# Performance work log

Hardware: AMD Instinct MI355X
Metric: run time of the kernel (lower is better)

Reference implementation:

```python
import jax, jax.numpy as jnp
import numpy as np

# Each of the 16 binary logic gates, relaxed to real values, is a multilinear
# function: gate(a,b) = c0 + c1*a + c2*b + c3*a*b. Rows follow the standard
# difflogic ordering: FALSE, AND, a&~b, a, ~a&b, b, XOR, OR, NOR, XNOR,
# ~b, a|~b, ~a, ~a|b, NAND, TRUE.
GATE_COEF = jnp.array([
    [0.0,  0.0,  0.0,  0.0],   # 0:  false
    [0.0,  0.0,  0.0,  1.0],   # 1:  a AND b
    [0.0,  1.0,  0.0, -1.0],   # 2:  a AND NOT b
    [0.0,  1.0,  0.0,  0.0],   # 3:  a
    [0.0,  0.0,  1.0, -1.0],   # 4:  NOT a AND b
    [0.0,  0.0,  1.0,  0.0],   # 5:  b
    [0.0,  1.0,  1.0, -2.0],   # 6:  a XOR b
    [0.0,  1.0,  1.0, -1.0],   # 7:  a OR b
    [1.0, -1.0, -1.0,  1.0],   # 8:  NOR
    [1.0, -1.0, -1.0,  2.0],   # 9:  XNOR
    [1.0,  0.0, -1.0,  0.0],   # 10: NOT b
    [1.0,  0.0, -1.0,  1.0],   # 11: a OR NOT b
    [1.0, -1.0,  0.0,  0.0],   # 12: NOT a
    [1.0, -1.0,  0.0,  1.0],   # 13: NOT a OR b
    [1.0,  0.0,  0.0, -1.0],   # 14: NAND
    [1.0,  0.0,  0.0,  0.0],   # 15: true
], dtype=jnp.float32)

B, IN_DIM, HIDDEN, N_LAYERS, OUT_DIM, TAU = 4096, 1024, 8192, 6, 8, 10.0
NPO = HIDDEN // OUT_DIM  # neurons_per_output


def logic_layer(h, w, ia, ib):
    # h: [B, in_dim]; w: [H, 16]; ia, ib: [H] int indices into in_dim.
    # Softmax-weighted blend of 16 gates == multilinear form with blended coefs.
    p = jax.nn.softmax(w, axis=-1)          # [H, 16]
    c = p @ GATE_COEF                       # [H, 4]
    a = h[:, ia]                            # [B, H] gather
    b = h[:, ib]                            # [B, H] gather
    return c[:, 0] + c[:, 1] * a + c[:, 2] * b + c[:, 3] * (a * b)


def setup_inputs() -> dict:
    key = jax.random.key(0)
    ks = jax.random.split(key, 8)
    return {
        "x": jax.random.uniform(ks[0], (B, IN_DIM), dtype=jnp.float32),
        "logic_w": jax.random.normal(ks[1], (N_LAYERS, HIDDEN, 16), dtype=jnp.float32),
        "scaler_w": jax.random.normal(ks[2], (OUT_DIM, OUT_DIM), dtype=jnp.float32) * 0.1,
        "scaler_b": jax.random.normal(ks[3], (OUT_DIM,), dtype=jnp.float32) * 0.1,
        "idx0_a": jax.random.randint(ks[4], (HIDDEN,), 0, IN_DIM, dtype=jnp.int32),
        "idx0_b": jax.random.randint(ks[5], (HIDDEN,), 0, IN_DIM, dtype=jnp.int32),
        "idx_a": jax.random.randint(ks[6], (N_LAYERS - 1, HIDDEN), 0, HIDDEN, dtype=jnp.int32),
        "idx_b": jax.random.randint(ks[7], (N_LAYERS - 1, HIDDEN), 0, HIDDEN, dtype=jnp.int32),
    }


def reference(x, logic_w, scaler_w, scaler_b, idx0_a, idx0_b, idx_a, idx_b):
    h = (x.reshape(x.shape[0], -1) > 0.5).astype(jnp.float32)   # binarize
    h = logic_layer(h, logic_w[0], idx0_a, idx0_b)               # [B, HIDDEN]
    for i in range(N_LAYERS - 1):
        h = logic_layer(h, logic_w[i + 1], idx_a[i], idx_b[i])
    h = h.reshape(h.shape[0], OUT_DIM, NPO)                      # [B, O, NPO]
    values = jnp.sum(h, axis=2) / TAU                            # [B, O]
    q_values = values @ scaler_w.T + scaler_b                    # nn.Linear
    return q_values
```

## Files before the change

kernel.cpp:

```cpp
#include <hip/hip_runtime.h>
#include <hip/hip_fp16.h>

constexpr int BATCH    = 4096;
constexpr int IN_DIM   = 1024;
constexpr int HIDDEN   = 8192;
constexpr int N_LAYERS = 6;
constexpr int OUT_DIM  = 8;
constexpr float INV_TAU = 0.1f;

constexpr int TB   = 4;
constexpr int NTH  = 1024;
constexpr int NPT  = HIDDEN / NTH;
constexpr int NWAVES = NTH / 64;

__device__ __forceinline__ uint2 pack4(float4 v) {
    __half2 lo = __float22half2_rn(make_float2(v.x, v.y));
    __half2 hi = __float22half2_rn(make_float2(v.z, v.w));
    uint2 r;
    r.x = *(const unsigned int*)&lo;
    r.y = *(const unsigned int*)&hi;
    return r;
}
__device__ __forceinline__ float4 unpack4(uint2 p) {
    __half2 lo = *(const __half2*)&p.x;
    __half2 hi = *(const __half2*)&p.y;
    float2 a = __half22float2(lo);
    float2 b = __half22float2(hi);
    return make_float4(a.x, a.y, b.x, b.y);
}

__global__ void prep_kernel(const float* __restrict__ logic_w,
                            const int* __restrict__ idx0_a,
                            const int* __restrict__ idx0_b,
                            const int* __restrict__ idx_a,
                            const int* __restrict__ idx_b,
                            uint2* __restrict__ coefp,
                            unsigned int* __restrict__ idxp, int n)
{
    int id = blockIdx.x * blockDim.x + threadIdx.x;
    if (id >= n) return;
    const int l = id / HIDDEN;
    const int j = id - l * HIDDEN;

    int ia, ib;
    if (l == 0) { ia = idx0_a[j]; ib = idx0_b[j]; }
    else        { ia = idx_a[(size_t)(l - 1) * HIDDEN + j];
                  ib = idx_b[(size_t)(l - 1) * HIDDEN + j]; }
    idxp[id] = (unsigned int)ia | ((unsigned int)ib << 16);

    const float4* w4 = (const float4*)(logic_w + (size_t)id * 16);
    float4 wa = w4[0], wb = w4[1], wc = w4[2], wd = w4[3];
    float wv[16] = {wa.x, wa.y, wa.z, wa.w, wb.x, wb.y, wb.z, wb.w,
                    wc.x, wc.y, wc.z, wc.w, wd.x, wd.y, wd.z, wd.w};
    float m = wv[0];
#pragma unroll
    for (int i = 1; i < 16; ++i) m = fmaxf(m, wv[i]);
    float e[16];
    float s = 0.f;
#pragma unroll
    for (int i = 0; i < 16; ++i) { e[i] = expf(wv[i] - m); s += e[i]; }
    float inv = 1.f / s;
    const float G0[16] = {0,0,0,0,0,0,0,0, 1,1,1,1,1,1,1,1};
    const float G1[16] = {0,0,1,1,0,0,1,1, -1,-1,0,0,-1,-1,0,0};
    const float G2[16] = {0,0,0,0,1,1,1,1, -1,-1,-1,-1,0,0,0,0};
    const float G3[16] = {0,1,-1,0,-1,0,-2,-1, 1,2,0,1,0,1,-1,0};
    float c0 = 0.f, c1 = 0.f, c2 = 0.f, c3 = 0.f;
#pragma unroll
    for (int i = 0; i < 16; ++i) {
        float p = e[i] * inv;
        c0 = fmaf(p, G0[i], c0);
        c1 = fmaf(p, G1[i], c1);
        c2 = fmaf(p, G2[i], c2);
        c3 = fmaf(p, G3[i], c3);
    }
    coefp[id] = pack4(make_float4(c0, c1, c2, c3));
}

__device__ __forceinline__ float4 gate4(float4 a, float4 b, float4 c) {
    float4 r;
    r.x = fmaf(c.w, a.x * b.x, fmaf(c.z, b.x, fmaf(c.y, a.x, c.x)));
    r.y = fmaf(c.w, a.y * b.y, fmaf(c.z, b.y, fmaf(c.y, a.y, c.x)));
    r.z = fmaf(c.w, a.z * b.z, fmaf(c.z, b.z, fmaf(c.y, a.z, c.x)));
    r.w = fmaf(c.w, a.w * b.w, fmaf(c.z, b.w, fmaf(c.y, a.w, c.x)));
    return r;
}

__global__ __launch_bounds__(NTH) void net_kernel(
    const float*  __restrict__ x,
    const uint2*  __restrict__ coefp,
    const unsigned int* __restrict__ idxp,
    const float*  __restrict__ scaler_w, const float* __restrict__ scaler_b,
    float* __restrict__ out)
{
    __shared__ uint2 h[HIDDEN];
    __shared__ uint2 hx[IN_DIM];
    __shared__ float4 warr[NWAVES];
    __shared__ float  vals[TB][OUT_DIM];

    const int tid = threadIdx.x;
    const int b0  = blockIdx.x * TB;

    {
        float4 xv;
        xv.x = (x[(size_t)(b0 + 0) * IN_DIM + tid] > 0.5f) ? 1.f : 0.f;
        xv.y = (x[(size_t)(b0 + 1) * IN_DIM + tid] > 0.5f) ? 1.f : 0.f;
        xv.z = (x[(size_t)(b0 + 2) * IN_DIM + tid] > 0.5f) ? 1.f : 0.f;
        xv.w = (x[(size_t)(b0 + 3) * IN_DIM + tid] > 0.5f) ? 1.f : 0.f;
        hx[tid] = pack4(xv);
    }
    __syncthreads();

    uint2 acc[NPT];

#pragma unroll
    for (int k = 0; k < NPT; ++k) {
        int j = k * NTH + tid;
        unsigned int pr = idxp[j];
        float4 a = unpack4(hx[pr & 0xffffu]);
        float4 b = unpack4(hx[pr >> 16]);
        float4 c = unpack4(coefp[j]);
        acc[k] = pack4(gate4(a, b, c));
    }
#pragma unroll
    for (int k = 0; k < NPT; ++k) h[k * NTH + tid] = acc[k];
    __syncthreads();

    for (int l = 1; l < N_LAYERS; ++l) {
        const unsigned int* ip = idxp  + (size_t)l * HIDDEN;
        const uint2*        cp = coefp + (size_t)l * HIDDEN;
#pragma unroll
        for (int k = 0; k < NPT; ++k) {
            int j = k * NTH + tid;
            unsigned int pr = ip[j];
            float4 a = unpack4(h[pr & 0xffffu]);
            float4 b = unpack4(h[pr >> 16]);
            float4 c = unpack4(cp[j]);
            acc[k] = pack4(gate4(a, b, c));
        }
        __syncthreads();
#pragma unroll
        for (int k = 0; k < NPT; ++k) h[k * NTH + tid] = acc[k];
        __syncthreads();
    }

    {
        const int k    = tid >> 7;
        const int base = k * 1024 + (tid & 127);
        float4 v = make_float4(0.f, 0.f, 0.f, 0.f);
#pragma unroll
        for (int i = 0; i < 8; ++i) {
            float4 t = unpack4(h[base + 128 * i]);
            v.x += t.x; v.y += t.y; v.z += t.z; v.w += t.w;
        }
#pragma unroll
        for (int off = 32; off > 0; off >>= 1) {
            v.x += __shfl_down(v.x, off);
            v.y += __shfl_down(v.y, off);
            v.z += __shfl_down(v.z, off);
            v.w += __shfl_down(v.w, off);
        }
        if ((tid & 63) == 0) warr[tid >> 6] = v;
    }
    __syncthreads();
    if (tid < OUT_DIM) {
        float4 a = warr[2 * tid], b = warr[2 * tid + 1];
        vals[0][tid] = (a.x + b.x) * INV_TAU;
        vals[1][tid] = (a.y + b.y) * INV_TAU;
        vals[2][tid] = (a.z + b.z) * INV_TAU;
        vals[3][tid] = (a.w + b.w) * INV_TAU;
    }
    __syncthreads();
    if (tid < TB * OUT_DIM) {
        int t  = tid >> 3;
        int oo = tid & 7;
        float q = scaler_b[oo];
#pragma unroll
        for (int o2 = 0; o2 < OUT_DIM; ++o2)
            q = fmaf(vals[t][o2], scaler_w[oo * OUT_DIM + o2], q);
        out[(size_t)(b0 + t) * OUT_DIM + oo] = q;
    }
}

extern "C" void kernel_launch(void* const* d_in, const int* in_sizes, int n_in,
                              void* d_out, int out_size, void* d_ws, size_t ws_size,
                              hipStream_t stream)
{
    const float* x        = (const float*)d_in[0];
    const float* logic_w  = (const float*)d_in[1];
    const float* scaler_w = (const float*)d_in[2];
    const float* scaler_b = (const float*)d_in[3];
    const int*   idx0_a   = (const int*)d_in[4];
    const int*   idx0_b   = (const int*)d_in[5];
    const int*   idx_a    = (const int*)d_in[6];
    const int*   idx_b    = (const int*)d_in[7];
    float* out = (float*)d_out;

    const int n = N_LAYERS * HIDDEN;
    uint2*        coefp = (uint2*)d_ws;
    unsigned int* idxp  = (unsigned int*)((char*)d_ws + (size_t)n * sizeof(uint2));

    prep_kernel<<<(n + 255) / 256, 256, 0, stream>>>(logic_w, idx0_a, idx0_b,
                                                     idx_a, idx_b, coefp, idxp, n);
    net_kernel<<<BATCH / TB, NTH, 0, stream>>>(x, coefp, idxp,
                                               scaler_w, scaler_b, out);
}
```

Before: 129.4 us.

## Compute gates in packed half2 and assign contiguous neurons per thread with vector loads

Measured after the change: 131.0 us. Within noise of the previous version (+1.2%).

```diff
diff --git a/kernel.cpp b/kernel.cpp
--- a/kernel.cpp
+++ b/kernel.cpp
@@ -13,19 +13,21 @@
 constexpr int NPT  = HIDDEN / NTH;
 constexpr int NWAVES = NTH / 64;
 
+__device__ __forceinline__ __half2 u2h(unsigned int u) {
+    union { unsigned int u; __half2 h; } v; v.u = u; return v.h;
+}
+__device__ __forceinline__ unsigned int h2u(__half2 h) {
+    union { unsigned int u; __half2 h; } v; v.h = h; return v.u;
+}
+
 __device__ __forceinline__ uint2 pack4(float4 v) {
     __half2 lo = __float22half2_rn(make_float2(v.x, v.y));
     __half2 hi = __float22half2_rn(make_float2(v.z, v.w));
-    uint2 r;
-    r.x = *(const unsigned int*)&lo;
-    r.y = *(const unsigned int*)&hi;
-    return r;
+    uint2 r; r.x = h2u(lo); r.y = h2u(hi); return r;
 }
 __device__ __forceinline__ float4 unpack4(uint2 p) {
-    __half2 lo = *(const __half2*)&p.x;
-    __half2 hi = *(const __half2*)&p.y;
-    float2 a = __half22float2(lo);
-    float2 b = __half22float2(hi);
+    float2 a = __half22float2(u2h(p.x));
+    float2 b = __half22float2(u2h(p.y));
     return make_float4(a.x, a.y, b.x, b.y);
 }
 
@@ -76,13 +78,15 @@
     coefp[id] = pack4(make_float4(c0, c1, c2, c3));
 }
 
-__device__ __forceinline__ float4 gate4(float4 a, float4 b, float4 c) {
-    float4 r;
-    r.x = fmaf(c.w, a.x * b.x, fmaf(c.z, b.x, fmaf(c.y, a.x, c.x)));
-    r.y = fmaf(c.w, a.y * b.y, fmaf(c.z, b.y, fmaf(c.y, a.y, c.x)));
-    r.z = fmaf(c.w, a.z * b.z, fmaf(c.z, b.z, fmaf(c.y, a.z, c.x)));
-    r.w = fmaf(c.w, a.w * b.w, fmaf(c.z, b.w, fmaf(c.y, a.w, c.x)));
-    return r;
+__device__ __forceinline__ uint2 gateh(uint2 a, uint2 b, uint2 c) {
+    __half2 cp01 = u2h(c.x), cp23 = u2h(c.y);
+    __half2 c0 = __low2half2(cp01), c1 = __high2half2(cp01);
+    __half2 c2 = __low2half2(cp23), c3 = __high2half2(cp23);
+    __half2 alo = u2h(a.x), ahi = u2h(a.y);
+    __half2 blo = u2h(b.x), bhi = u2h(b.y);
+    __half2 rlo = __hfma2(blo, __hfma2(c3, alo, c2), __hfma2(c1, alo, c0));
+    __half2 rhi = __hfma2(bhi, __hfma2(c3, ahi, c2), __hfma2(c1, ahi, c0));
+    uint2 r; r.x = h2u(rlo); r.y = h2u(rhi); return r;
 }
 
 __global__ __launch_bounds__(NTH) void net_kernel(
@@ -111,35 +115,46 @@
     __syncthreads();
 
     uint2 acc[NPT];
-
-#pragma unroll
-    for (int k = 0; k < NPT; ++k) {
-        int j = k * NTH + tid;
-        unsigned int pr = idxp[j];
-        float4 a = unpack4(hx[pr & 0xffffu]);
-        float4 b = unpack4(hx[pr >> 16]);
-        float4 c = unpack4(coefp[j]);
-        acc[k] = pack4(gate4(a, b, c));
-    }
-#pragma unroll
-    for (int k = 0; k < NPT; ++k) h[k * NTH + tid] = acc[k];
+    const int jb = tid * NPT;
+
+    {
+        const uint4* ip4 = (const uint4*)(idxp + jb);
+        const uint4* cp4 = (const uint4*)(coefp + jb);
+        uint4 ix[2] = {ip4[0], ip4[1]};
+        uint4 cf[4] = {cp4[0], cp4[1], cp4[2], cp4[3]};
+        const unsigned int* prs = (const unsigned int*)ix;
+        const uint2*        cs  = (const uint2*)cf;
+#pragma unroll
+        for (int k = 0; k < NPT; ++k) {
+            unsigned int pr = prs[k];
+            acc[k] = gateh(hx[pr & 0xffffu], hx[pr >> 16], cs[k]);
+        }
+    }
+    {
+        uint4* hw = (uint4*)(h + jb);
+#pragma unroll
+        for (int k = 0; k < NPT / 2; ++k)
+            hw[k] = make_uint4(acc[2*k].x, acc[2*k].y, acc[2*k+1].x, acc[2*k+1].y);
+    }
     __syncthreads();
 
     for (int l = 1; l < N_LAYERS; ++l) {
-        const unsigned int* ip = idxp  + (size_t)l * HIDDEN;
-        const uint2*        cp = coefp + (size_t)l * HIDDEN;
+        const uint4* ip4 = (const uint4*)(idxp  + (size_t)l * HIDDEN + jb);
+        const uint4* cp4 = (const uint4*)(coefp + (size_t)l * HIDDEN + jb);
+        uint4 ix[2] = {ip4[0], ip4[1]};
+        uint4 cf[4] = {cp4[0], cp4[1], cp4[2], cp4[3]};
+        const unsigned int* prs = (const unsigned int*)ix;
+        const uint2*        cs  = (const uint2*)cf;
 #pragma unroll
         for (int k = 0; k < NPT; ++k) {
-            int j = k * NTH + tid;
-            unsigned int pr = ip[j];
-            float4 a = unpack4(h[pr & 0xffffu]);
-            float4 b = unpack4(h[pr >> 16]);
-            float4 c = unpack4(cp[j]);
-            acc[k] = pack4(gate4(a, b, c));
+            unsigned int pr = prs[k];
+            acc[k] = gateh(h[pr & 0xffffu], h[pr >> 16], cs[k]);
         }
         __syncthreads();
-#pragma unroll
-        for (int k = 0; k < NPT; ++k) h[k * NTH + tid] = acc[k];
+        uint4* hw = (uint4*)(h + jb);
+#pragma unroll
+        for (int k = 0; k < NPT / 2; ++k)
+            hw[k] = make_uint4(acc[2*k].x, acc[2*k].y, acc[2*k+1].x, acc[2*k+1].y);
         __syncthreads();
     }
 
```
